# Optimization experiments

Hardware: AMD Instinct MI355X
Metric: run time of the kernel (lower is better)

The kernel has to match this reference:

```python
import jax, jax.numpy as jnp
import numpy as np

N_IN = 50000
N_OUT = 50000
DEG = 16
E = N_OUT * DEG
C = 64
F = 64


def cartesian_to_spherical(cart, extents):
    # cart: [E,3]
    r_plane_2 = cart[..., 0] ** 2 + cart[..., 1] ** 2
    r_2 = r_plane_2 + cart[..., 2] ** 2
    r_safe = jnp.maximum(jnp.sqrt(r_2), 1e-10)
    cos_phi = cart[..., 2] / r_safe
    r_plane_safe = jnp.maximum(jnp.sqrt(r_plane_2), 1e-10)
    sin_theta = cart[..., 1] / r_plane_safe
    cos_theta = cart[..., 0] / r_plane_safe
    r_normalized = r_safe / extents
    return jnp.stack([r_normalized, cos_phi, sin_theta, cos_theta], axis=-1)  # [E,4]


def setup_inputs() -> dict:
    key = jax.random.key(0)
    k1, k2, k3, k4, k5 = jax.random.split(key, 5)
    input_features = jax.random.normal(k1, (N_IN, C), dtype=jnp.float32)
    input_positions = jax.random.uniform(k2, (N_IN, 3), dtype=jnp.float32)
    output_positions = jax.random.uniform(k3, (N_OUT, 3), dtype=jnp.float32)
    extents = jnp.ones((1,), dtype=jnp.float32)
    kernel = jax.random.normal(k4, (4, C, F), dtype=jnp.float32) * (1.0 / np.sqrt(C))
    bias = jnp.zeros((F,), dtype=jnp.float32)
    neighbors_index = jax.random.randint(k5, (E,), 0, N_IN, dtype=jnp.int32)
    neighbors_row_splits = (DEG * jnp.arange(N_OUT + 1)).astype(jnp.int32)
    return {
        "input_features": input_features,
        "input_positions": input_positions,
        "output_positions": output_positions,
        "extents": extents,
        "kernel": kernel,
        "bias": bias,
        "neighbors_index": neighbors_index,
        "neighbors_row_splits": neighbors_row_splits,
    }


def reference(input_features, input_positions, output_positions, extents,
              kernel, bias, neighbors_index, neighbors_row_splits):
    n_out = output_positions.shape[0]
    n_edges = neighbors_index.shape[0]
    counts = neighbors_row_splits[1:] - neighbors_row_splits[:-1]  # [N_out]
    # segment id of each edge (which output point it belongs to)
    seg_ids = jnp.repeat(jnp.arange(n_out), counts, total_repeat_length=n_edges)
    expanded_query = output_positions[seg_ids]                     # [E,3]
    difference = input_positions[neighbors_index] - expanded_query  # [E,3]
    sph = cartesian_to_spherical(difference, extents)              # [E,4]
    neighbors_feats = input_features[neighbors_index]              # [E,C]
    # contract features with kernel over C first -> [E,4,F] (avoids [E,C,F])
    tmp = jnp.einsum('ec,scf->esf', neighbors_feats, kernel)
    out_edge = jnp.einsum('es,esf->ef', sph, tmp)                  # [E,F]
    out_features = jax.ops.segment_sum(out_edge, seg_ids, num_segments=n_out)
    out_features = out_features + bias
    return out_features
```

## Files before the change

kernel.cpp:

```cpp
#include <hip/hip_runtime.h>

typedef unsigned short u16;
typedef __attribute__((ext_vector_type(8))) short bf16x8;
typedef __attribute__((ext_vector_type(8))) unsigned short u16x8;
typedef __attribute__((ext_vector_type(4))) float f32x4;

#define TPS   4
#define BLOCK (TPS * 2 * 64)

__device__ __forceinline__ float bf2f(u16 u) {
    union { unsigned i; float f; } v; v.i = (unsigned)u << 16; return v.f;
}
__device__ __forceinline__ u16 f2bf(float f) {
    union { float f; unsigned u; } v; v.f = f;
    unsigned r = v.u + 0x7fff + ((v.u >> 16) & 1);
    return (u16)(r >> 16);
}

__global__ __launch_bounds__(256)
void prep_all(const float* __restrict__ feats, const float* __restrict__ kmat,
              u16* __restrict__ fbf, u16* __restrict__ kbg, int n8) {
    const int id = blockIdx.x * 256 + threadIdx.x;
    if (id < n8) {
        const float4 a = ((const float4*)feats)[2 * id];
        const float4 b = ((const float4*)feats)[2 * id + 1];
        union { u16 h[8]; int4 v; } p;
        p.h[0] = f2bf(a.x); p.h[1] = f2bf(a.y); p.h[2] = f2bf(a.z); p.h[3] = f2bf(a.w);
        p.h[4] = f2bf(b.x); p.h[5] = f2bf(b.y); p.h[6] = f2bf(b.z); p.h[7] = f2bf(b.w);
        ((int4*)fbf)[id] = p.v;
    }
    if (id < 16384) {
        const int k = id >> 6, n = id & 63;
        const int kstep = k >> 5, quad = (k >> 3) & 3, j = k & 7;
        const int ntile = n >> 4, lanep = (quad << 4) | (n & 15);
        kbg[((((ntile << 3) | kstep) << 6) | lanep) * 8 + j] = f2bf(kmat[id]);
    }
}

template<bool WS>
__global__ __launch_bounds__(BLOCK)
void sphconv_ksplit(const float* __restrict__ featsf,
                    const u16* __restrict__ fbf,
                    const u16* __restrict__ kbg,
                    const float* __restrict__ in_pos,
                    const float* __restrict__ out_pos,
                    const float* __restrict__ extents,
                    const float* __restrict__ kmat,
                    const float* __restrict__ bias,
                    const int* __restrict__ nidx,
                    const int* __restrict__ rsplits,
                    float* __restrict__ out,
                    int n_out, int ntiles, int n_edges)
{
    __shared__ u16 KB[16384];
    __shared__ int idxT[TPS][16][16];
    __shared__ _Float16 sphT[TPS][16][16][4];

    const int tid = threadIdx.x, wave = tid >> 6, lane = tid & 63;
    const int ts = wave >> 1;
    const int kh = wave & 1;

    if constexpr (WS) {
        const int4* s = (const int4*)kbg; int4* d = (int4*)KB;
        #pragma unroll
        for (int i = 0; i < 4; ++i) d[tid + (i << 9)] = s[tid + (i << 9)];
    } else {
        for (int i = tid; i < 16384; i += BLOCK) {
            const int n = i & 63, k = i >> 6;
            const int kstep = k >> 5, quad = (k >> 3) & 3, j = k & 7;
            const int ntile = n >> 4, lanep = (quad << 4) | (n & 15);
            KB[((((ntile << 3) | kstep) << 6) | lanep) * 8 + j] = f2bf(kmat[i]);
        }
    }

    const int tile = blockIdx.x * TPS + ts;
    const int tile_c = min(tile, ntiles - 1);
    const int obase = tile_c << 4;
    const int m = lane & 15, quad = lane >> 4;

    const float inv_ext = __fdividef(1.f, extents[0]);

    #pragma unroll
    for (int u = 0; u < 2; ++u) {
        const int slot = (kh << 7) | (u << 6) | lane;
        const int mm = slot >> 4, t = slot & 15;
        const int o  = obase + mm;
        const int oc = min(o, n_out - 1);
        const int e0 = rsplits[oc], e1 = rsplits[oc + 1];
        const int e  = e0 + t;
        const bool v = (o < n_out) && (e < e1);
        const int id = nidx[min(e, n_edges - 1)];
        const float dx = in_pos[id * 3 + 0] - out_pos[oc * 3 + 0];
        const float dy = in_pos[id * 3 + 1] - out_pos[oc * 3 + 1];
        const float dz = in_pos[id * 3 + 2] - out_pos[oc * 3 + 2];
        const float rp2 = dx * dx + dy * dy;
        const float r2  = rp2 + dz * dz;
        const float rs  = fmaxf(sqrtf(r2), 1e-10f);
        const float rp  = fmaxf(sqrtf(rp2), 1e-10f);
        const float ir  = __fdividef(1.f, rs);
        const float irp = __fdividef(1.f, rp);
        union { _Float16 hh[4]; short4 s4; } pk;
        pk.hh[0] = (_Float16)(v ? rs * inv_ext : 0.f);
        pk.hh[1] = (_Float16)(v ? dz * ir      : 0.f);
        pk.hh[2] = (_Float16)(v ? dy * irp     : 0.f);
        pk.hh[3] = (_Float16)(v ? dx * irp     : 0.f);
        idxT[ts][t][mm] = id;
        *(short4*)&sphT[ts][t][mm][0] = pk.s4;
    }
    __syncthreads();

    float acc[4][8];
    #pragma unroll
    for (int s = 0; s < 4; ++s)
        #pragma unroll
        for (int j = 0; j < 8; ++j) acc[s][j] = 0.f;

    int idx_r[16];
    #pragma unroll
    for (int t = 0; t < 16; ++t) idx_r[t] = idxT[ts][t][m];

    #pragma unroll 8
    for (int t = 0; t < 16; ++t) {
        union { short4 s4; _Float16 hh[4]; } up;
        up.s4 = *(const short4*)&sphT[ts][t][m][0];
        float fv[8];
        if constexpr (WS) {
            const u16x8 f0 = *(const u16x8*)(fbf + (idx_r[t] << 6) + (kh << 5) + (quad << 3));
            #pragma unroll
            for (int j = 0; j < 8; ++j) fv[j] = bf2f(f0[j]);
        } else {
            const float* fr = featsf + (idx_r[t] << 6) + (kh << 5) + (quad << 3);
            const float4 a0 = *(const float4*)fr;
            const float4 a1 = *(const float4*)(fr + 4);
            fv[0] = a0.x; fv[1] = a0.y; fv[2] = a0.z; fv[3] = a0.w;
            fv[4] = a1.x; fv[5] = a1.y; fv[6] = a1.z; fv[7] = a1.w;
        }
        #pragma unroll
        for (int s = 0; s < 4; ++s) {
            const float w = (float)up.hh[s];
            #pragma unroll
            for (int j = 0; j < 8; ++j)
                acc[s][j] = fmaf(w, fv[j], acc[s][j]);
        }
    }

    bf16x8 afr[4];
    #pragma unroll
    for (int s = 0; s < 4; ++s) {
        union { u16 hh[8]; bf16x8 v; } p;
        #pragma unroll
        for (int j = 0; j < 8; ++j) p.hh[j] = f2bf(acc[s][j]);
        afr[s] = p.v;
    }

    f32x4 C[4] = {{0,0,0,0},{0,0,0,0},{0,0,0,0},{0,0,0,0}};
    const bf16x8* kbp = (const bf16x8*)KB;
    #pragma unroll
    for (int nt = 0; nt < 4; ++nt)
        #pragma unroll
        for (int s = 0; s < 4; ++s) {
            const int ks = (s << 1) | kh;
            const bf16x8 b = kbp[(((nt << 3) | ks) << 6) | lane];
            C[nt] = __builtin_amdgcn_mfma_f32_16x16x32_bf16(afr[s], b, C[nt], 0, 0, 0);
        }

    f32x4* redp = (f32x4*)sphT;
    const bool store_ok = (tile < ntiles);
    __syncthreads();
    if (kh == 1) {
        redp[((ts << 1) | 0) * 64 + lane] = C[0];
        redp[((ts << 1) | 1) * 64 + lane] = C[1];
    }
    __syncthreads();
    if (kh == 0 && store_ok) {
        #pragma unroll
        for (int nt = 0; nt < 2; ++nt) {
            const f32x4 P = redp[((ts << 1) | nt) * 64 + lane];
            const int f = (nt << 4) | m;
            const float bv = bias[f];
            #pragma unroll
            for (int r = 0; r < 4; ++r) {
                const int oo = obase + (quad << 2) + r;
                if (oo < n_out) out[(oo << 6) | f] = C[nt][r] + P[r] + bv;
            }
        }
    }
    __syncthreads();
    if (kh == 1) {
        redp[((ts << 1) | 0) * 64 + lane] = C[2];
        redp[((ts << 1) | 1) * 64 + lane] = C[3];
    }
    __syncthreads();
    if (kh == 0 && store_ok) {
        #pragma unroll
        for (int nt = 2; nt < 4; ++nt) {
            const f32x4 P = redp[((ts << 1) | (nt - 2)) * 64 + lane];
            const int f = (nt << 4) | m;
            const float bv = bias[f];
            #pragma unroll
            for (int r = 0; r < 4; ++r) {
                const int oo = obase + (quad << 2) + r;
                if (oo < n_out) out[(oo << 6) | f] = C[nt][r] + P[r] + bv;
            }
        }
    }
}

extern "C" void kernel_launch(void* const* d_in, const int* in_sizes, int n_in,
                              void* d_out, int out_size, void* d_ws, size_t ws_size,
                              hipStream_t stream) {
    const float* feats   = (const float*)d_in[0];
    const float* in_pos  = (const float*)d_in[1];
    const float* out_pos = (const float*)d_in[2];
    const float* extents = (const float*)d_in[3];
    const float* kmat    = (const float*)d_in[4];
    const float* bias    = (const float*)d_in[5];
    const int*   nidx    = (const int*)d_in[6];
    const int*   rsplits = (const int*)d_in[7];
    const int n_out   = in_sizes[7] - 1;
    const int n_edges = in_sizes[6];
    const int ntiles  = (n_out + 15) >> 4;
    const int grid    = (ntiles + TPS - 1) / TPS;

    const size_t fbf_bytes = (size_t)in_sizes[0] * 2;
    const size_t need = fbf_bytes + 32768;
    if (ws_size >= need && (in_sizes[0] & 7) == 0) {
        u16* fbf = (u16*)d_ws;
        u16* kbg = (u16*)((char*)d_ws + fbf_bytes);
        const int n8 = in_sizes[0] / 8;
        const int pmax = n8 > 16384 ? n8 : 16384;
        prep_all<<<(pmax + 255) / 256, 256, 0, stream>>>(feats, kmat, fbf, kbg, n8);
        sphconv_ksplit<true><<<grid, BLOCK, 0, stream>>>(
            feats, fbf, kbg, in_pos, out_pos, extents, kmat, bias, nidx, rsplits,
            (float*)d_out, n_out, ntiles, n_edges);
    } else {
        sphconv_ksplit<false><<<grid, BLOCK, 0, stream>>>(
            feats, nullptr, nullptr, in_pos, out_pos, extents, kmat, bias, nidx, rsplits,
            (float*)d_out, n_out, ntiles, n_edges);
    }
}
```

Baseline: 111.2 us.

## Drop shared-memory kernel staging; one tile per 128-thread block, B from global

Each block now handles a single 16-output tile with two k-half waves, not four tiles. The 32KB shared-memory copy of the bf16 kernel matrix is removed, and MFMA B fragments are read straight from the global/L2 prepacked buffer. This removes the per-block LDS fill and its barrier, shrinks LDS use so more blocks fit per CU, and cuts the reduction to a single sync. In exchange, every wave rereads kernel fragments from cache, and there are four times as many blocks.

```diff
diff --git a/kernel.cpp b/kernel.cpp
--- a/kernel.cpp
+++ b/kernel.cpp
@@ -5,8 +5,7 @@
 typedef __attribute__((ext_vector_type(8))) unsigned short u16x8;
 typedef __attribute__((ext_vector_type(4))) float f32x4;
 
-#define TPS   4
-#define BLOCK (TPS * 2 * 64)
+#define BLOCK 128
 
 __device__ __forceinline__ float bf2f(u16 u) {
     union { unsigned i; float f; } v; v.i = (unsigned)u << 16; return v.f;
@@ -39,50 +38,34 @@
 
 template<bool WS>
 __global__ __launch_bounds__(BLOCK)
-void sphconv_ksplit(const float* __restrict__ featsf,
-                    const u16* __restrict__ fbf,
-                    const u16* __restrict__ kbg,
-                    const float* __restrict__ in_pos,
-                    const float* __restrict__ out_pos,
-                    const float* __restrict__ extents,
-                    const float* __restrict__ kmat,
-                    const float* __restrict__ bias,
-                    const int* __restrict__ nidx,
-                    const int* __restrict__ rsplits,
-                    float* __restrict__ out,
-                    int n_out, int ntiles, int n_edges)
+void sphconv_tile(const float* __restrict__ featsf,
+                  const u16* __restrict__ fbf,
+                  const u16* __restrict__ kbg,
+                  const float* __restrict__ in_pos,
+                  const float* __restrict__ out_pos,
+                  const float* __restrict__ extents,
+                  const float* __restrict__ kmat,
+                  const float* __restrict__ bias,
+                  const int* __restrict__ nidx,
+                  const int* __restrict__ rsplits,
+                  float* __restrict__ out,
+                  int n_out, int n_edges)
 {
-    __shared__ u16 KB[16384];
-    __shared__ int idxT[TPS][16][16];
-    __shared__ _Float16 sphT[TPS][16][16][4];
-
-    const int tid = threadIdx.x, wave = tid >> 6, lane = tid & 63;
-    const int ts = wave >> 1;
-    const int kh = wave & 1;
-
-    if constexpr (WS) {
-        const int4* s = (const int4*)kbg; int4* d = (int4*)KB;
-        #pragma unroll
-        for (int i = 0; i < 4; ++i) d[tid + (i << 9)] = s[tid + (i << 9)];
-    } else {
-        for (int i = tid; i < 16384; i += BLOCK) {
-            const int n = i & 63, k = i >> 6;
-            const int kstep = k >> 5, quad = (k >> 3) & 3, j = k & 7;
-            const int ntile = n >> 4, lanep = (quad << 4) | (n & 15);
-            KB[((((ntile << 3) | kstep) << 6) | lanep) * 8 + j] = f2bf(kmat[i]);
-        }
-    }
-
-    const int tile = blockIdx.x * TPS + ts;
-    const int tile_c = min(tile, ntiles - 1);
-    const int obase = tile_c << 4;
+    __shared__ _Float16 sphT[16][16][4];
+    __shared__ int      idxT[16][16];
+    __shared__ __align__(16) float redT[4][64][4];
+
+    const int tid = threadIdx.x;
+    const int kh  = tid >> 6;
+    const int lane = tid & 63;
     const int m = lane & 15, quad = lane >> 4;
+    const int obase = blockIdx.x << 4;
 
     const float inv_ext = __fdividef(1.f, extents[0]);
 
     #pragma unroll
     for (int u = 0; u < 2; ++u) {
-        const int slot = (kh << 7) | (u << 6) | lane;
+        const int slot = (u << 7) | tid;
         const int mm = slot >> 4, t = slot & 15;
         const int o  = obase + mm;
         const int oc = min(o, n_out - 1);
@@ -104,8 +87,8 @@
         pk.hh[1] = (_Float16)(v ? dz * ir      : 0.f);
         pk.hh[2] = (_Float16)(v ? dy * irp     : 0.f);
         pk.hh[3] = (_Float16)(v ? dx * irp     : 0.f);
-        idxT[ts][t][mm] = id;
-        *(short4*)&sphT[ts][t][mm][0] = pk.s4;
+        idxT[t][mm] = id;
+        *(short4*)&sphT[t][mm][0] = pk.s4;
     }
     __syncthreads();
 
@@ -115,21 +98,18 @@
         #pragma unroll
         for (int j = 0; j < 8; ++j) acc[s][j] = 0.f;
 
-    int idx_r[16];
-    #pragma unroll
-    for (int t = 0; t < 16; ++t) idx_r[t] = idxT[ts][t][m];
-
-    #pragma unroll 8
+    #pragma unroll 4
     for (int t = 0; t < 16; ++t) {
+        const int idx = idxT[t][m];
         union { short4 s4; _Float16 hh[4]; } up;
-        up.s4 = *(const short4*)&sphT[ts][t][m][0];
+        up.s4 = *(const short4*)&sphT[t][m][0];
         float fv[8];
         if constexpr (WS) {
-            const u16x8 f0 = *(const u16x8*)(fbf + (idx_r[t] << 6) + (kh << 5) + (quad << 3));
+            const u16x8 f0 = *(const u16x8*)(fbf + (idx << 6) + (kh << 5) + (quad << 3));
             #pragma unroll
             for (int j = 0; j < 8; ++j) fv[j] = bf2f(f0[j]);
         } else {
-            const float* fr = featsf + (idx_r[t] << 6) + (kh << 5) + (quad << 3);
+            const float* fr = featsf + (idx << 6) + (kh << 5) + (quad << 3);
             const float4 a0 = *(const float4*)fr;
             const float4 a1 = *(const float4*)(fr + 4);
             fv[0] = a0.x; fv[1] = a0.y; fv[2] = a0.z; fv[3] = a0.w;
@@ -154,47 +134,40 @@
     }
 
     f32x4 C[4] = {{0,0,0,0},{0,0,0,0},{0,0,0,0},{0,0,0,0}};
-    const bf16x8* kbp = (const bf16x8*)KB;
-    #pragma unroll
-    for (int nt = 0; nt < 4; ++nt)
+    #pragma unroll
+    for (int nt = 0; nt < 4; ++nt) {
+        bf16x8 b[4];
         #pragma unroll
         for (int s = 0; s < 4; ++s) {
             const int ks = (s << 1) | kh;
-            const bf16x8 b = kbp[(((nt << 3) | ks) << 6) | lane];
-            C[nt] = __builtin_amdgcn_mfma_f32_16x16x32_bf16(afr[s], b, C[nt], 0, 0, 0);
-        }
-
-    f32x4* redp = (f32x4*)sphT;
-    const bool store_ok = (tile < ntiles);
+            if constexpr (WS) {
+                b[s] = *(const bf16x8*)(kbg + ((((nt << 3) | ks) << 6) | lane) * 8);
+            } else {
+                union { u16 hh[8]; bf16x8 v; } p;
+                #pragma unroll
+                for (int j = 0; j < 8; ++j) {
+                    const int k = (ks << 5) | (quad << 3) | j;
+                    const int n = (nt << 4) | m;
+                    p.hh[j] = f2bf(kmat[k * 64 + n]);
+                }
+                b[s] = p.v;
+            }
+        }
+        #pragma unroll
+        for (int s = 0; s < 4; ++s)
+            C[nt] = __builtin_amdgcn_mfma_f32_16x16x32_bf16(afr[s], b[s], C[nt], 0, 0, 0);
+    }
+
+    if (kh == 1) {
+        #pragma unroll
+        for (int nt = 0; nt < 4; ++nt)
+            *(f32x4*)&redT[nt][lane][0] = C[nt];
+    }
     __syncthreads();
-    if (kh == 1) {
-        redp[((ts << 1) | 0) * 64 + lane] = C[0];
-        redp[((ts << 1) | 1) * 64 + lane] = C[1];
-    }
-    __syncthreads();
-    if (kh == 0 && store_ok) {
-        #pragma unroll
-        for (int nt = 0; nt < 2; ++nt) {
-            const f32x4 P = redp[((ts << 1) | nt) * 64 + lane];
-            const int f = (nt << 4) | m;
-            const float bv = bias[f];
-            #pragma unroll
-            for (int r = 0; r < 4; ++r) {
-                const int oo = obase + (quad << 2) + r;
-                if (oo < n_out) out[(oo << 6) | f] = C[nt][r] + P[r] + bv;
-            }
-        }
-    }
-    __syncthreads();
-    if (kh == 1) {
-        redp[((ts << 1) | 0) * 64 + lane] = C[2];
-        redp[((ts << 1) | 1) * 64 + lane] = C[3];
-    }
-    __syncthreads();
-    if (kh == 0 && store_ok) {
-        #pragma unroll
-        for (int nt = 2; nt < 4; ++nt) {
-            const f32x4 P = redp[((ts << 1) | (nt - 2)) * 64 + lane];
+    if (kh == 0) {
+        #pragma unroll
+        for (int nt = 0; nt < 4; ++nt) {
+            const f32x4 P = *(const f32x4*)&redT[nt][lane][0];
             const int f = (nt << 4) | m;
             const float bv = bias[f];
             #pragma unroll
@@ -220,7 +193,6 @@
     const int n_out   = in_sizes[7] - 1;
     const int n_edges = in_sizes[6];
     const int ntiles  = (n_out + 15) >> 4;
-    const int grid    = (ntiles + TPS - 1) / TPS;
 
     const size_t fbf_bytes = (size_t)in_sizes[0] * 2;
     const size_t need = fbf_bytes + 32768;
@@ -230,12 +202,12 @@
         const int n8 = in_sizes[0] / 8;
         const int pmax = n8 > 16384 ? n8 : 16384;
         prep_all<<<(pmax + 255) / 256, 256, 0, stream>>>(feats, kmat, fbf, kbg, n8);
-        sphconv_ksplit<true><<<grid, BLOCK, 0, stream>>>(
+        sphconv_tile<true><<<ntiles, BLOCK, 0, stream>>>(
             feats, fbf, kbg, in_pos, out_pos, extents, kmat, bias, nidx, rsplits,
-            (float*)d_out, n_out, ntiles, n_edges);
+            (float*)d_out, n_out, n_edges);
     } else {
-        sphconv_ksplit<false><<<grid, BLOCK, 0, stream>>>(
+        sphconv_tile<false><<<ntiles, BLOCK, 0, stream>>>(
             feats, nullptr, nullptr, in_pos, out_pos, extents, kmat, bias, nidx, rsplits,
-            (float*)d_out, n_out, ntiles, n_edges);
-    }
-}
+            (float*)d_out, n_out, n_edges);
+    }
+}
```

Result: faster. 107.5 us (-3.3%).
